# Optimization experiments

Measured on AMD Instinct MI355X. Metric: run time of the kernel, lower is better.

The kernel has to match this reference:

```python
import jax, jax.numpy as jnp
import numpy as np

NH = 8
DIM = 512
NP = 1024
MNP = 4096
BS = 4
TOPK = 32


def setup_inputs() -> dict:
    key = jax.random.key(0)
    ks = jax.random.split(key, 10)
    q = jax.random.normal(ks[0], (NP, BS, DIM), dtype=jnp.float32)
    k = jax.random.normal(ks[1], (MNP, BS, DIM), dtype=jnp.float32)
    v = jax.random.normal(ks[2], (MNP, BS, DIM), dtype=jnp.float32)
    rns_indices = jax.random.randint(ks[3], (BS, NP, TOPK), 0, MNP)
    s = 0.02
    W1 = jax.random.normal(ks[4], (DIM, DIM), dtype=jnp.float32) * s
    b1 = jnp.zeros((DIM,), dtype=jnp.float32)
    W2 = jax.random.normal(ks[5], (DIM, DIM), dtype=jnp.float32) * s
    b2 = jnp.zeros((DIM,), dtype=jnp.float32)
    W3 = jax.random.normal(ks[6], (DIM, DIM), dtype=jnp.float32) * s
    b3 = jnp.zeros((DIM,), dtype=jnp.float32)
    return {"q": q, "k": k, "v": v, "rns_indices": rns_indices,
            "W1": W1, "b1": b1, "W2": W2, "b2": b2, "W3": W3, "b3": b3}


def reference(q, k, v, rns_indices, W1, b1, W2, b2, W3, b3):
    np_, bs, dim = q.shape
    mnp = k.shape[0]
    nh = NH
    dh = dim // nh
    # seq-first -> batch-first, linear projections (torch Linear: x @ W.T + b)
    qh = (jnp.einsum('nbd,ed->bne', q, W1) + b1).reshape(bs, np_, nh, dh)
    kh = (jnp.einsum('mbd,ed->bme', k, W2) + b2).reshape(bs, mnp, nh, dh)
    vh = (jnp.einsum('mbd,ed->bme', v, W3) + b3).reshape(bs, mnp, nh, dh)
    # dense scores: [bs, nh, np, mnp]
    w = jnp.einsum('bnhd,bmhd->bhnm', qh, kh) / jnp.sqrt(jnp.asarray(dh, w_dtype := qh.dtype))
    # scatter-built neighbor mask: [bs, np, mnp] (shared across heads)
    b_idx = jnp.arange(bs)[:, None, None]
    n_idx = jnp.arange(np_)[None, :, None]
    mask = jnp.zeros((bs, np_, mnp), dtype=w.dtype).at[b_idx, n_idx, rns_indices].set(1.0)
    mask = mask[:, None, :, :]  # broadcast over heads
    w = w * mask + (-1e9) * (1.0 - mask)
    w = jax.nn.softmax(w, axis=3)
    out = jnp.einsum('bhnm,bmhd->nbhd', w, vh).reshape(np_, bs, dim)
    return out
```

## Files before the change

kernel.cpp:

```cpp
#include <hip/hip_runtime.h>
#include <stdint.h>

#define NH   8
#define DIM  512
#define NP   1024
#define MNP  4096
#define BS   4
#define TOPK 32
#define DH   64

typedef unsigned short u16;
typedef __attribute__((ext_vector_type(8))) short bf16x8;
typedef __attribute__((ext_vector_type(4))) float f32x4;

__device__ __forceinline__ u16 f2bf(float f) {
    union { float f; unsigned u; } x; x.f = f;
    unsigned r = x.u + 0x7FFFu + ((x.u >> 16) & 1u);
    return (u16)(r >> 16);
}
__device__ __forceinline__ float bf2f(u16 h) {
    union { unsigned u; float f; } x; x.u = ((unsigned)h) << 16;
    return x.f;
}

__device__ __forceinline__ void async16(const void* g, void* l) {
    __builtin_amdgcn_global_load_lds(
        (const __attribute__((address_space(1))) unsigned int*)g,
        (__attribute__((address_space(3))) unsigned int*)l, 16, 0, 0);
}

__global__ void cvt_all(const float* __restrict__ W1, const float* __restrict__ W2,
                        const float* __restrict__ W3, const float* __restrict__ q,
                        const float* __restrict__ k,  const float* __restrict__ v,
                        u16* __restrict__ wall, u16* __restrict__ act) {
    const size_t base = ((size_t)blockIdx.x * 256 + threadIdx.x) * 4;
    const size_t gstride = (size_t)4800 * 256 * 4;
#pragma unroll
    for (int g = 0; g < 4; g++) {
        size_t i = base + (size_t)g * gstride;
        const float* s; u16* d;
        if (i < 786432) {
            d = wall + i;
            s = (i < 262144) ? W1 + i : (i < 524288) ? W2 + (i - 262144) : W3 + (i - 524288);
        } else {
            size_t j = i - 786432;
            d = act + j;
            s = (j < 2097152) ? q + j : (j < 10485760) ? k + (j - 2097152) : v + (j - 10485760);
        }
        float4 val = *(const float4*)s;
        ushort4 o;
        o.x = f2bf(val.x); o.y = f2bf(val.y); o.z = f2bf(val.z); o.w = f2bf(val.w);
        *(ushort4*)d = o;
    }
}

__global__ __launch_bounds__(256, 2)
void proj_gemm(const u16* __restrict__ act, const u16* __restrict__ wall,
               const float* __restrict__ b1, const float* __restrict__ b2,
               const float* __restrict__ b3, u16* __restrict__ outall) {
    __shared__ u16 As[2][128 * 64];
    __shared__ u16 Bs[2][128 * 64];

    const int bid = blockIdx.x;
    const int x = bid / 288;
    const int t = bid % 288;
    int z, y;
    if (t < 32)       { z = 0; y = t; }
    else if (t < 160) { z = 1; y = t - 32; }
    else              { z = 2; y = t - 160; }

    const size_t aoff = (z == 0) ? 0u : (z == 1) ? 2097152u : 10485760u;
    const u16* A = act + aoff;
    const u16* W = wall + (size_t)z * 262144;
    const float* bias = (z == 0) ? b1 : (z == 1) ? b2 : b3;
    u16* C = outall + aoff;

    const int tid  = threadIdx.x;
    const int bm   = y * 128;
    const int bn   = x * 128;
    const int wave = tid >> 6;
    const int lane = tid & 63;
    const int wm   = (wave & 1) * 64;
    const int wn   = (wave >> 1) * 64;
    const int l16  = lane & 15;
    const int quad = lane >> 4;

    const int srow = lane >> 3;
    const int scol = ((lane & 7) ^ srow) * 8;

    const int lrow = wave * 32;
    const u16* Ag = A + (size_t)(bm + lrow + srow) * 512 + scol;
    const u16* Wg = W + (size_t)(bn + lrow + srow) * 512 + scol;

    f32x4 acc[4][4] = {};

    #define STAGE(buf, k0)                                                     \
        _Pragma("unroll")                                                      \
        for (int r = 0; r < 4; r++) {                                          \
            async16(Ag + (size_t)(r * 8) * 512 + (k0),                         \
                    &As[buf][(lrow + r * 8) * 64 + lane * 8]);                 \
            async16(Wg + (size_t)(r * 8) * 512 + (k0),                         \
                    &Bs[buf][(lrow + r * 8) * 64 + lane * 8]);                 \
        }

    STAGE(0, 0);
    __syncthreads();

#pragma unroll
    for (int kt = 0; kt < 8; kt++) {
        const int cur = kt & 1;
        if (kt < 7) { STAGE(cur ^ 1, (kt + 1) * 64); }
#pragma unroll
        for (int kk = 0; kk < 64; kk += 32) {
            bf16x8 af[4], bfr[4];
            const int g = (kk >> 3) + quad;
#pragma unroll
            for (int i = 0; i < 4; i++) {
                int ra = wm + i * 16 + l16;
                int rb = wn + i * 16 + l16;
                af[i]  = *(const bf16x8*)(&As[cur][ra * 64 + ((g ^ (ra & 7)) << 3)]);
                bfr[i] = *(const bf16x8*)(&Bs[cur][rb * 64 + ((g ^ (rb & 7)) << 3)]);
            }
#pragma unroll
            for (int i = 0; i < 4; i++)
#pragma unroll
                for (int j = 0; j < 4; j++)
                    acc[i][j] = __builtin_amdgcn_mfma_f32_16x16x32_bf16(
                        af[i], bfr[j], acc[i][j], 0, 0, 0);
        }
        __syncthreads();
    }
    #undef STAGE

#pragma unroll
    for (int i = 0; i < 4; i++) {
        int row = bm + wm + i * 16 + quad * 4;
#pragma unroll
        for (int j = 0; j < 4; j++) {
            int col = bn + wn + j * 16 + l16;
            float bv = bias[col];
#pragma unroll
            for (int r = 0; r < 4; r++)
                C[(size_t)(row + r) * 512 + col] = f2bf(acc[i][j][r] + bv);
        }
    }
}

__global__ __launch_bounds__(256)
void attn_kernel(const u16* __restrict__ Qh, const u16* __restrict__ Kh,
                 const u16* __restrict__ Vh, const int* __restrict__ rns,
                 float* __restrict__ out) {
    __shared__ float sq[4][512];
    __shared__ float swt[4][32 * 9];
    __shared__ int   srw[4][TOPK];

    const int wv   = threadIdx.x >> 6;
    const int lane = threadIdx.x & 63;
    const int pair = blockIdx.x * 4 + wv;
    const int n = pair >> 2;
    const int b = pair & 3;
    const int s   = lane >> 1;
    const int sub = lane & 1;

    int myidx = rns[(b * NP + n) * TOPK + s];
    int myrow = (myidx * BS + b) * DIM;
    if (sub == 0) srw[wv][s] = myrow;

    bool dup = false;
#pragma unroll
    for (int j = 0; j < TOPK; j++) {
        int other = __shfl(myidx, j * 2, 64);
        dup = dup || ((j < s) && (other == myidx));
    }

    {
        const u16* qrow = Qh + (size_t)pair * DIM;
        uint4 qv = *(const uint4*)(qrow + lane * 8);
        float4 f0 = { bf2f((u16)qv.x), bf2f((u16)(qv.x >> 16)),
                      bf2f((u16)qv.y), bf2f((u16)(qv.y >> 16)) };
        float4 f1 = { bf2f((u16)qv.z), bf2f((u16)(qv.z >> 16)),
                      bf2f((u16)qv.w), bf2f((u16)(qv.w >> 16)) };
        *(float4*)(&sq[wv][lane * 8])     = f0;
        *(float4*)(&sq[wv][lane * 8 + 4]) = f1;
    }
    __builtin_amdgcn_wave_barrier();

    const float* qw = sq[wv];
    float sc[NH];
#pragma unroll
    for (int h = 0; h < NH; h++) {
        const u16* kp = Kh + myrow + h * DH + sub * 32;
        const float* qp = qw + h * DH + sub * 32;
        float acc = 0.f;
#pragma unroll
        for (int d = 0; d < 32; d += 8) {
            uint4 kv = *(const uint4*)(kp + d);
            acc += qp[d + 0] * bf2f((u16)kv.x) + qp[d + 1] * bf2f((u16)(kv.x >> 16))
                 + qp[d + 2] * bf2f((u16)kv.y) + qp[d + 3] * bf2f((u16)(kv.y >> 16))
                 + qp[d + 4] * bf2f((u16)kv.z) + qp[d + 5] * bf2f((u16)(kv.z >> 16))
                 + qp[d + 6] * bf2f((u16)kv.w) + qp[d + 7] * bf2f((u16)(kv.w >> 16));
        }
        sc[h] = acc;
    }
#pragma unroll
    for (int h = 0; h < NH; h++) {
        sc[h] += __shfl_xor(sc[h], 1, 64);
        sc[h] = dup ? -1e30f : sc[h] * 0.125f;
    }
    float w[NH];
#pragma unroll
    for (int h = 0; h < NH; h++) {
        float m = sc[h];
        m = fmaxf(m, __shfl_xor(m, 2, 64));
        m = fmaxf(m, __shfl_xor(m, 4, 64));
        m = fmaxf(m, __shfl_xor(m, 8, 64));
        m = fmaxf(m, __shfl_xor(m, 16, 64));
        m = fmaxf(m, __shfl_xor(m, 32, 64));
        float e = __expf(sc[h] - m);
        float t = e;
        t += __shfl_xor(t, 2, 64);
        t += __shfl_xor(t, 4, 64);
        t += __shfl_xor(t, 8, 64);
        t += __shfl_xor(t, 16, 64);
        t += __shfl_xor(t, 32, 64);
        w[h] = e / t;
    }
    if (sub == 0) {
#pragma unroll
        for (int h = 0; h < NH; h++) swt[wv][s * 9 + h] = w[h];
    }
    __builtin_amdgcn_wave_barrier();

    const int h  = lane >> 3;
    const int e8 = lane * 8;
    float a[8] = {0, 0, 0, 0, 0, 0, 0, 0};
#pragma unroll 8
    for (int si = 0; si < TOPK; si++) {
        int   row = srw[wv][si];
        float wgt = swt[wv][si * 9 + h];
        uint4 vv = *(const uint4*)(Vh + row + e8);
        a[0] += wgt * bf2f((u16)vv.x); a[1] += wgt * bf2f((u16)(vv.x >> 16));
        a[2] += wgt * bf2f((u16)vv.y); a[3] += wgt * bf2f((u16)(vv.y >> 16));
        a[4] += wgt * bf2f((u16)vv.z); a[5] += wgt * bf2f((u16)(vv.z >> 16));
        a[6] += wgt * bf2f((u16)vv.w); a[7] += wgt * bf2f((u16)(vv.w >> 16));
    }
    float* op = out + (size_t)pair * DIM + e8;
    float4 o0 = {a[0], a[1], a[2], a[3]};
    float4 o1 = {a[4], a[5], a[6], a[7]};
    *(float4*)op       = o0;
    *((float4*)op + 1) = o1;
}

extern "C" void kernel_launch(void* const* d_in, const int* in_sizes, int n_in,
                              void* d_out, int out_size, void* d_ws, size_t ws_size,
                              hipStream_t stream) {
    const float* q  = (const float*)d_in[0];
    const float* k  = (const float*)d_in[1];
    const float* v  = (const float*)d_in[2];
    const int* rns  = (const int*)d_in[3];
    const float* W1 = (const float*)d_in[4];
    const float* b1 = (const float*)d_in[5];
    const float* W2 = (const float*)d_in[6];
    const float* b2 = (const float*)d_in[7];
    const float* W3 = (const float*)d_in[8];
    const float* b3 = (const float*)d_in[9];
    float* out = (float*)d_out;

    u16* ws   = (u16*)d_ws;
    u16* wall = ws;
    u16* act  = wall + 786432;
    u16* proj = act + 18874368;
    u16* Qh = proj;
    u16* Kh = proj + 2097152;
    u16* Vh = proj + 10485760;

    cvt_all<<<4800, 256, 0, stream>>>(W1, W2, W3, q, k, v, wall, act);
    proj_gemm<<<1152, 256, 0, stream>>>(act, wall, b1, b2, b3, proj);
    attn_kernel<<<NP * BS / 4, 256, 0, stream>>>(Qh, Kh, Vh, rns, out);
}
```

Measured before the change: 189.4 us.

## Fuse fp32-to-bf16 conversion into projection GEMM tile loads

Removes the separate conversion kernel and has the projection GEMM read fp32 activations and weights directly. Each tile is loaded into registers, packed to bf16 with v_cvt_pk_bf16_f32, and written to swizzled LDS, with the next tile's global loads issued before the MFMA loop. This drops one kernel launch and a full write and re-read of a bf16 copy of all inputs. In exchange the async global-to-LDS path is replaced by register staging, which raises register pressure, and weights are now converted redundantly by every block.

```diff
diff --git a/kernel.cpp b/kernel.cpp
--- a/kernel.cpp
+++ b/kernel.cpp
@@ -22,40 +22,16 @@
     union { unsigned u; float f; } x; x.u = ((unsigned)h) << 16;
     return x.f;
 }
-
-__device__ __forceinline__ void async16(const void* g, void* l) {
-    __builtin_amdgcn_global_load_lds(
-        (const __attribute__((address_space(1))) unsigned int*)g,
-        (__attribute__((address_space(3))) unsigned int*)l, 16, 0, 0);
-}
-
-__global__ void cvt_all(const float* __restrict__ W1, const float* __restrict__ W2,
-                        const float* __restrict__ W3, const float* __restrict__ q,
-                        const float* __restrict__ k,  const float* __restrict__ v,
-                        u16* __restrict__ wall, u16* __restrict__ act) {
-    const size_t base = ((size_t)blockIdx.x * 256 + threadIdx.x) * 4;
-    const size_t gstride = (size_t)4800 * 256 * 4;
-#pragma unroll
-    for (int g = 0; g < 4; g++) {
-        size_t i = base + (size_t)g * gstride;
-        const float* s; u16* d;
-        if (i < 786432) {
-            d = wall + i;
-            s = (i < 262144) ? W1 + i : (i < 524288) ? W2 + (i - 262144) : W3 + (i - 524288);
-        } else {
-            size_t j = i - 786432;
-            d = act + j;
-            s = (j < 2097152) ? q + j : (j < 10485760) ? k + (j - 2097152) : v + (j - 10485760);
-        }
-        float4 val = *(const float4*)s;
-        ushort4 o;
-        o.x = f2bf(val.x); o.y = f2bf(val.y); o.z = f2bf(val.z); o.w = f2bf(val.w);
-        *(ushort4*)d = o;
-    }
+__device__ __forceinline__ unsigned cvt_pk_bf16(float a, float b) {
+    unsigned r;
+    asm("v_cvt_pk_bf16_f32 %0, %1, %2" : "=v"(r) : "v"(a), "v"(b));
+    return r;
 }
 
 __global__ __launch_bounds__(256, 2)
-void proj_gemm(const u16* __restrict__ act, const u16* __restrict__ wall,
+void proj_gemm(const float* __restrict__ qf, const float* __restrict__ kf,
+               const float* __restrict__ vf, const float* __restrict__ W1,
+               const float* __restrict__ W2, const float* __restrict__ W3,
                const float* __restrict__ b1, const float* __restrict__ b2,
                const float* __restrict__ b3, u16* __restrict__ outall) {
     __shared__ u16 As[2][128 * 64];
@@ -69,11 +45,11 @@
     else if (t < 160) { z = 1; y = t - 32; }
     else              { z = 2; y = t - 160; }
 
-    const size_t aoff = (z == 0) ? 0u : (z == 1) ? 2097152u : 10485760u;
-    const u16* A = act + aoff;
-    const u16* W = wall + (size_t)z * 262144;
+    const float* Asrc = (z == 0) ? qf : (z == 1) ? kf : vf;
+    const float* Wsrc = (z == 0) ? W1 : (z == 1) ? W2 : W3;
     const float* bias = (z == 0) ? b1 : (z == 1) ? b2 : b3;
-    u16* C = outall + aoff;
+    const size_t coff = (z == 0) ? 0u : (z == 1) ? 2097152u : 10485760u;
+    u16* C = outall + coff;
 
     const int tid  = threadIdx.x;
     const int bm   = y * 128;
@@ -85,31 +61,44 @@
     const int l16  = lane & 15;
     const int quad = lane >> 4;
 
-    const int srow = lane >> 3;
-    const int scol = ((lane & 7) ^ srow) * 8;
-
-    const int lrow = wave * 32;
-    const u16* Ag = A + (size_t)(bm + lrow + srow) * 512 + scol;
-    const u16* Wg = W + (size_t)(bn + lrow + srow) * 512 + scol;
+    const int sr = tid >> 4;
+    const int fi = tid & 15;
+    const int gq = fi >> 1;
+    const int hf = fi & 1;
+    const int ldst = sr * 64 + ((gq ^ (sr & 7)) << 3) + hf * 4;
+
+    const float* Ab = Asrc + (size_t)(bm + sr) * 512 + fi * 4;
+    const float* Wb = Wsrc + (size_t)(bn + sr) * 512 + fi * 4;
+
+    float4 av[8], wv[8];
+
+    #define LOADT(k0)                                                          \
+        _Pragma("unroll")                                                      \
+        for (int s = 0; s < 8; s++) {                                          \
+            av[s] = *(const float4*)(Ab + (size_t)s * 8192 + (k0));            \
+            wv[s] = *(const float4*)(Wb + (size_t)s * 8192 + (k0));            \
+        }
+    #define WRITET(buf)                                                        \
+        _Pragma("unroll")                                                      \
+        for (int s = 0; s < 8; s++) {                                          \
+            uint2 pa = { cvt_pk_bf16(av[s].x, av[s].y),                        \
+                         cvt_pk_bf16(av[s].z, av[s].w) };                      \
+            uint2 pw = { cvt_pk_bf16(wv[s].x, wv[s].y),                        \
+                         cvt_pk_bf16(wv[s].z, wv[s].w) };                      \
+            *(uint2*)&As[buf][ldst + s * 1024] = pa;                           \
+            *(uint2*)&Bs[buf][ldst + s * 1024] = pw;                           \
+        }
 
     f32x4 acc[4][4] = {};
 
-    #define STAGE(buf, k0)                                                     \
-        _Pragma("unroll")                                                      \
-        for (int r = 0; r < 4; r++) {                                          \
-            async16(Ag + (size_t)(r * 8) * 512 + (k0),                         \
-                    &As[buf][(lrow + r * 8) * 64 + lane * 8]);                 \
-            async16(Wg + (size_t)(r * 8) * 512 + (k0),                         \
-                    &Bs[buf][(lrow + r * 8) * 64 + lane * 8]);                 \
-        }
-
-    STAGE(0, 0);
+    LOADT(0);
+    WRITET(0);
     __syncthreads();
 
 #pragma unroll
     for (int kt = 0; kt < 8; kt++) {
         const int cur = kt & 1;
-        if (kt < 7) { STAGE(cur ^ 1, (kt + 1) * 64); }
+        if (kt < 7) { LOADT((kt + 1) * 64); }
 #pragma unroll
         for (int kk = 0; kk < 64; kk += 32) {
             bf16x8 af[4], bfr[4];
@@ -128,9 +117,13 @@
                     acc[i][j] = __builtin_amdgcn_mfma_f32_16x16x32_bf16(
                         af[i], bfr[j], acc[i][j], 0, 0, 0);
         }
-        __syncthreads();
-    }
-    #undef STAGE
+        if (kt < 7) {
+            WRITET(cur ^ 1);
+            __syncthreads();
+        }
+    }
+    #undef LOADT
+    #undef WRITET
 
 #pragma unroll
     for (int i = 0; i < 4; i++) {
@@ -266,15 +259,11 @@
     const float* b3 = (const float*)d_in[9];
     float* out = (float*)d_out;
 
-    u16* ws   = (u16*)d_ws;
-    u16* wall = ws;
-    u16* act  = wall + 786432;
-    u16* proj = act + 18874368;
+    u16* proj = (u16*)d_ws;
     u16* Qh = proj;
     u16* Kh = proj + 2097152;
     u16* Vh = proj + 10485760;
 
-    cvt_all<<<4800, 256, 0, stream>>>(W1, W2, W3, q, k, v, wall, act);
-    proj_gemm<<<1152, 256, 0, stream>>>(act, wall, b1, b2, b3, proj);
+    proj_gemm<<<1152, 256, 0, stream>>>(q, k, v, W1, W2, W3, b1, b2, b3, proj);
     attn_kernel<<<NP * BS / 4, 256, 0, stream>>>(Qh, Kh, Vh, rns, out);
 }
```

Result: no change. 192.6 us (+1.7%).
